# Performance work log

Hardware: AMD Instinct MI355X
Metric: run time of the kernel (lower is better)

Reference implementation:

```python
import jax, jax.numpy as jnp
import numpy as np

D_MODEL = 1024
N_HEADS = 16
D_V = D_MODEL // N_HEADS  # 64; o_proj maps d_model -> d_v (quirk of the source)
B, S = 4, 2048


def setup_inputs() -> dict:
    key = jax.random.key(0)
    ks = jax.random.split(key, 5)
    scale = 1.0 / np.sqrt(D_MODEL)
    return {
        "in_features": jax.random.normal(ks[0], (B, S, D_MODEL), dtype=jnp.float32),
        "Wq": jax.random.normal(ks[1], (D_MODEL, D_MODEL), dtype=jnp.float32) * scale,
        "Wk": jax.random.normal(ks[2], (D_MODEL, D_MODEL), dtype=jnp.float32) * scale,
        "Wv": jax.random.normal(ks[3], (D_MODEL, D_MODEL), dtype=jnp.float32) * scale,
        "Wo": jax.random.normal(ks[4], (D_V, D_MODEL), dtype=jnp.float32) * scale,
    }


def reference(in_features, Wq, Wk, Wv, Wo):
    # Linear(in, out): y = x @ W^T, no bias. NOTE: source never splits heads;
    # attention runs single-head over the full d_model dims.
    Q = jnp.einsum('bsd,ed->bse', in_features, Wq)  # [B,S,D]
    K = jnp.einsum('bsd,ed->bse', in_features, Wk)
    V = jnp.einsum('bsd,ed->bse', in_features, Wv)

    scores = jnp.einsum('bqd,bkd->bqk', Q, K)       # [B,S,S]
    causal = jnp.tril(jnp.ones((S, S), dtype=bool))  # True = keep
    # source applies -inf mask BEFORE scaling (equivalent result)
    scores = jnp.where(causal[None, :, :], scores, -jnp.inf)
    scores = scores / jnp.sqrt(jnp.float32(D_MODEL))  # K.size(-1) == d_model
    attn = jax.nn.softmax(scores, axis=-1)
    ctx = jnp.einsum('bqk,bkd->bqd', attn, V)        # [B,S,D]
    return jnp.einsum('bsd,vd->bsv', ctx, Wo)        # [B,S,D_V]
```

## Files before the change

### kernel.cpp

```cpp
#include <hip/hip_runtime.h>
#include <math.h>

typedef unsigned short u16;
typedef unsigned int u32;
typedef __attribute__((ext_vector_type(8))) short short8;
typedef __attribute__((ext_vector_type(4))) short short4v;
typedef __attribute__((ext_vector_type(4))) float f32x4;

#define BB 4
#define SS 2048
#define DD 1024
#define DV 64
#define NYU 1152
#define BS (BB * SS)
#define SCALE (1.0f / 32.0f)

__device__ __forceinline__ u16 f2bf(float f) {
    u32 u = __builtin_bit_cast(u32, f);
    u32 r = u + 0x7fffu + ((u >> 16) & 1u);
    return (u16)(r >> 16);
}
__device__ __forceinline__ float bf2f(u16 b) {
    return __builtin_bit_cast(float, (u32)b << 16);
}
__device__ __forceinline__ void storeC(float* p, float v) { *p = v; }
__device__ __forceinline__ void storeC(u16* p, float v) { *p = f2bf(v); }

__global__ __launch_bounds__(256) void prep(const float* __restrict__ x,
                                            const float* __restrict__ Wq,
                                            const float* __restrict__ Wk,
                                            const float* __restrict__ Wo,
                                            const float* __restrict__ Wv,
                                            u16* __restrict__ x16,
                                            u16* __restrict__ Wqt,
                                            u16* __restrict__ Wkt,
                                            float* __restrict__ wpart) {
    __shared__ float smem[64 * 128];
    const int b = blockIdx.x;
    const int tid = threadIdx.x;
    if (b < 8192) {
        int i = b * 256 + tid;
        f32x4 v = ((const f32x4*)x)[i];
        short4v o;
        o.x = (short)f2bf(v.x); o.y = (short)f2bf(v.y);
        o.z = (short)f2bf(v.z); o.w = (short)f2bf(v.w);
        ((short4v*)x16)[i] = o;
    } else if (b < 8704) {
        const int bb = b - 8192;
        const float* src = (bb >> 8) ? Wk : Wq;
        u16* dst = (bb >> 8) ? Wkt : Wqt;
        const int rem = bb & 255;
        const int e0 = (rem >> 4) * 64, d0 = (rem & 15) * 64;
        u16* t = (u16*)smem;
        const int g = tid >> 6, lane = tid & 63;
        for (int r = g; r < 64; r += 4)
            t[r * 72 + lane] = f2bf(src[(size_t)(e0 + r) * DD + d0 + lane]);
        __syncthreads();
        for (int r = g; r < 64; r += 4)
            dst[(size_t)(d0 + r) * DD + e0 + lane] = t[lane * 72 + r];
    } else {
        const int bb = b - 8704;
        const int echunk = (bb & 7) * 128;
        const int kc = bb >> 3, kbase = kc * 128;
        for (int idx = tid; idx < 64 * 128; idx += 256)
            smem[idx] = Wo[(size_t)(idx >> 7) * DD + kbase + (idx & 127)];
        __syncthreads();
        const int eo = echunk + (tid & 31) * 4;
        const int ob = (tid >> 5) * 8;
        float acc[8][4] = {};
        for (int k = 0; k < 128; ++k) {
            f32x4 wv = *(const f32x4*)&Wv[(size_t)(kbase + k) * DD + eo];
#pragma unroll
            for (int oi = 0; oi < 8; ++oi) {
                float s = smem[(ob + oi) * 128 + k];
                acc[oi][0] += s * wv.x; acc[oi][1] += s * wv.y;
                acc[oi][2] += s * wv.z; acc[oi][3] += s * wv.w;
            }
        }
#pragma unroll
        for (int oi = 0; oi < 8; ++oi)
            *(f32x4*)&wpart[((size_t)kc * 64 + ob + oi) * DD + eo] =
                (f32x4){acc[oi][0], acc[oi][1], acc[oi][2], acc[oi][3]};
    }
}

__global__ __launch_bounds__(256) void reduce_all(const float* __restrict__ Gpart,
                                                  const float* __restrict__ wpart,
                                                  u16* __restrict__ Wall2) {
    const int bx = blockIdx.x;
    const int e0 = threadIdx.x * 4;
    f32x4 s = (f32x4){0.f, 0.f, 0.f, 0.f};
    if (bx < 1024) {
#pragma unroll
        for (int kc = 0; kc < 4; ++kc)
            s += *(const f32x4*)&Gpart[(size_t)kc * DD * DD + (size_t)bx * DD + e0];
    } else if (bx < 1088) {
#pragma unroll
        for (int kc = 0; kc < 8; ++kc)
            s += *(const f32x4*)&wpart[((size_t)kc * 64 + bx - 1024) * DD + e0];
    }
    short4v ov;
    ov.x = (short)f2bf(s.x); ov.y = (short)f2bf(s.y);
    ov.z = (short)f2bf(s.z); ov.w = (short)f2bf(s.w);
    *(short4v*)&Wall2[(size_t)bx * DD + e0] = ov;
}

template <int TM, int TN, int WM, int WN, typename OutT, int MODE>
__global__ __launch_bounds__(WM * WN * 64) void gemm_nt_mfma(
    const u16* __restrict__ A, const u16* __restrict__ B, OutT* __restrict__ C,
    int lda, int ldb, int ldc, int K, long sA, long sB, long sC) {
    constexpr int NW = WM * WN;
    constexpr int CA = TM / 16;
    constexpr int CB = TN / 16;

    const int z = blockIdx.z;
    A += (size_t)z * sA;
    B += (size_t)z * sB;
    C += (size_t)z * sC;
    int m0, n0;
    if constexpr (MODE == 3) {
        const int b = blockIdx.x;
        const int r = b & 7, q = b >> 3;
        m0 = (r * 8 + q / 9) * TM;
        n0 = (q % 9) * TN;
    } else {
        m0 = blockIdx.y * TM;
        n0 = blockIdx.x * TN;
    }

    __shared__ u16 As[TM * 32];
    __shared__ u16 Bs[TN * 32];

    const int tid = threadIdx.x;
    const int w = tid >> 6, lane = tid & 63;
    const int wm = w / WN, wn = w % WN;
    const int lrow = lane >> 2;
    const int lcol = (lane & 3) * 8;
    const int m16 = lane & 15;
    const int kh = (lane >> 4) * 8;

    f32x4 acc[4][4];
#pragma unroll
    for (int i = 0; i < 4; ++i)
#pragma unroll
        for (int j = 0; j < 4; ++j) acc[i][j] = (f32x4){0.f, 0.f, 0.f, 0.f};

    for (int k0 = 0; k0 < K; k0 += 32) {
        for (int c = w; c < CA; c += NW) {
            const u16* g = A + (size_t)(m0 + c * 16 + lrow) * lda + k0 + lcol;
            __builtin_amdgcn_global_load_lds(
                (const __attribute__((address_space(1))) void*)g,
                (__attribute__((address_space(3))) void*)(&As[c * 512]), 16, 0, 0);
        }
        for (int c = w; c < CB; c += NW) {
            const u16* g = B + (size_t)(n0 + c * 16 + lrow) * ldb + k0 + lcol;
            __builtin_amdgcn_global_load_lds(
                (const __attribute__((address_space(1))) void*)g,
                (__attribute__((address_space(3))) void*)(&Bs[c * 512]), 16, 0, 0);
        }
        __syncthreads();

        short8 a[4], b[4];
#pragma unroll
        for (int i = 0; i < 4; ++i)
            a[i] = *(const short8*)&As[(wm * 64 + i * 16 + m16) * 32 + kh];
#pragma unroll
        for (int j = 0; j < 4; ++j)
            b[j] = *(const short8*)&Bs[(wn * 64 + j * 16 + m16) * 32 + kh];
#pragma unroll
        for (int i = 0; i < 4; ++i)
#pragma unroll
            for (int j = 0; j < 4; ++j)
                acc[i][j] = __builtin_amdgcn_mfma_f32_16x16x32_bf16(a[i], b[j], acc[i][j], 0, 0, 0);
        __syncthreads();
    }

    const int crow0 = m0 + wm * 64 + (lane >> 4) * 4;
    const int ccol0 = n0 + wn * 64 + m16;
#pragma unroll
    for (int i = 0; i < 4; ++i)
#pragma unroll
        for (int j = 0; j < 4; ++j)
#pragma unroll
            for (int r = 0; r < 4; ++r)
                storeC(&C[(size_t)(crow0 + i * 16 + r) * ldc + ccol0 + j * 16],
                       acc[i][j][r]);
}

__global__ __launch_bounds__(256) void transpose_u(const u16* __restrict__ YU,
                                                   u16* __restrict__ Ut) {
    __shared__ u16 t[64][72];
    const int s0 = blockIdx.x * 64;
    const int g = threadIdx.x >> 6, lane = threadIdx.x & 63;
    for (int r = g; r < 64; r += 4)
        t[r][lane] = YU[(size_t)(s0 + r) * NYU + 1024 + lane];
    __syncthreads();
    for (int r = g; r < 64; r += 4)
        Ut[(size_t)r * BS + s0 + lane] = t[lane][r];
}

__global__ __launch_bounds__(256) void scores_pv(const u16* __restrict__ YU,
                                                 const u16* __restrict__ x16,
                                                 const u16* __restrict__ Ut,
                                                 float* __restrict__ out,
                                                 float* __restrict__ Lacc) {
    const int b = blockIdx.x;
    const int r8 = b & 7;
    const int z = r8 >> 1;
    const int t = 2 * (b >> 3) + (r8 & 1);
    int y = (int)((sqrtf(8.f * t + 1.f) - 1.f) * 0.5f);
    while ((y + 1) * (y + 2) / 2 <= t) ++y;
    while (y * (y + 1) / 2 > t) --y;
    const int m0 = y * 128;
    const int n0 = (t - y * (y + 1) / 2) * 128;

    const u16* A = YU + (size_t)z * SS * NYU;
    const u16* B = x16 + (size_t)z * SS * DD;

    __shared__ u16 As[128 * 32];
    __shared__ u16 Bs[128 * 32];
    __shared__ u16 Ps[128 * 136];

    const int tid = threadIdx.x;
    const int w = tid >> 6, lane = tid & 63;
    const int wm = w >> 1, wn = w & 1;
    const int lrow = lane >> 2;
    const int lcol = (lane & 3) * 8;
    const int m16 = lane & 15;
    const int kh = (lane >> 4) * 8;

    f32x4 acc[4][4];
#pragma unroll
    for (int i = 0; i < 4; ++i)
#pragma unroll
        for (int j = 0; j < 4; ++j) acc[i][j] = (f32x4){0.f, 0.f, 0.f, 0.f};

    for (int k0 = 0; k0 < DD; k0 += 32) {
        for (int c = w; c < 8; c += 4) {
            const u16* g = A + (size_t)(m0 + c * 16 + lrow) * NYU + k0 + lcol;
            __builtin_amdgcn_global_load_lds(
                (const __attribute__((address_space(1))) void*)g,
                (__attribute__((address_space(3))) void*)(&As[c * 512]), 16, 0, 0);
        }
        for (int c = w; c < 8; c += 4) {
            const u16* g = B + (size_t)(n0 + c * 16 + lrow) * DD + k0 + lcol;
            __builtin_amdgcn_global_load_lds(
                (const __attribute__((address_space(1))) void*)g,
                (__attribute__((address_space(3))) void*)(&Bs[c * 512]), 16, 0, 0);
        }
        __syncthreads();

        short8 a[4], bb[4];
#pragma unroll
        for (int i = 0; i < 4; ++i)
            a[i] = *(const short8*)&As[(wm * 64 + i * 16 + m16) * 32 + kh];
#pragma unroll
        for (int j = 0; j < 4; ++j)
            bb[j] = *(const short8*)&Bs[(wn * 64 + j * 16 + m16) * 32 + kh];
#pragma unroll
        for (int i = 0; i < 4; ++i)
#pragma unroll
            for (int j = 0; j < 4; ++j)
                acc[i][j] = __builtin_amdgcn_mfma_f32_16x16x32_bf16(a[i], bb[j], acc[i][j], 0, 0, 0);
        __syncthreads();
    }

    const int rl0 = wm * 64 + (lane >> 4) * 4;
    const int cl0 = wn * 64 + m16;
#pragma unroll
    for (int i = 0; i < 4; ++i)
#pragma unroll
        for (int j = 0; j < 4; ++j)
#pragma unroll
            for (int r = 0; r < 4; ++r) {
                const int rl = rl0 + i * 16 + r;
                const int cl = cl0 + j * 16;
                float p = __expf(acc[i][j][r] * SCALE);
                Ps[rl * 136 + cl] = (n0 + cl <= m0 + rl) ? f2bf(p) : (u16)0;
            }
    __syncthreads();

    short8 ones8;
#pragma unroll
    for (int e = 0; e < 8; ++e) ones8[e] = (short)0x3F80;

    const u16* Utz = Ut + (size_t)z * SS + n0;
    f32x4 accO[2][4], accL[2];
#pragma unroll
    for (int i = 0; i < 2; ++i) {
        accL[i] = (f32x4){0.f, 0.f, 0.f, 0.f};
#pragma unroll
        for (int j = 0; j < 4; ++j) accO[i][j] = (f32x4){0.f, 0.f, 0.f, 0.f};
    }
#pragma unroll
    for (int ks = 0; ks < 4; ++ks) {
        const int k0 = ks * 32;
        short8 a[2], bb[4];
#pragma unroll
        for (int i = 0; i < 2; ++i)
            a[i] = *(const short8*)&Ps[(w * 32 + i * 16 + m16) * 136 + k0 + kh];
#pragma unroll
        for (int j = 0; j < 4; ++j)
            bb[j] = *(const short8*)&Utz[(size_t)(j * 16 + m16) * BS + k0 + kh];
#pragma unroll
        for (int i = 0; i < 2; ++i) {
#pragma unroll
            for (int j = 0; j < 4; ++j)
                accO[i][j] = __builtin_amdgcn_mfma_f32_16x16x32_bf16(a[i], bb[j], accO[i][j], 0, 0, 0);
            accL[i] = __builtin_amdgcn_mfma_f32_16x16x32_bf16(a[i], ones8, accL[i], 0, 0, 0);
        }
    }

    float* Oz = out + (size_t)z * SS * DV;
    float* Lz = Lacc + (size_t)z * SS;
    const int wrow = m0 + w * 32 + (lane >> 4) * 4;
#pragma unroll
    for (int i = 0; i < 2; ++i) {
#pragma unroll
        for (int j = 0; j < 4; ++j)
#pragma unroll
            for (int r = 0; r < 4; ++r)
                atomicAdd(&Oz[(size_t)(wrow + i * 16 + r) * DV + j * 16 + m16],
                          accO[i][j][r]);
        if (m16 == 0)
#pragma unroll
            for (int r = 0; r < 4; ++r)
                atomicAdd(&Lz[wrow + i * 16 + r], accL[i][r]);
    }
}

__global__ __launch_bounds__(256) void normalize(float* __restrict__ out,
                                                 const float* __restrict__ Lacc) {
    int i = blockIdx.x * 256 + threadIdx.x;
    f32x4 v = ((f32x4*)out)[i];
    const float inv = 1.f / Lacc[(i * 4) >> 6];
    v.x *= inv; v.y *= inv; v.z *= inv; v.w *= inv;
    ((f32x4*)out)[i] = v;
}

extern "C" void kernel_launch(void* const* d_in, const int* in_sizes, int n_in,
                              void* d_out, int out_size, void* d_ws, size_t ws_size,
                              hipStream_t stream) {
    const float* x  = (const float*)d_in[0];
    const float* Wq = (const float*)d_in[1];
    const float* Wk = (const float*)d_in[2];
    const float* Wv = (const float*)d_in[3];
    const float* Wo = (const float*)d_in[4];
    float* out = (float*)d_out;

    u16* x16   = (u16*)d_ws;
    u16* Wqt16 = x16 + (size_t)BB * SS * DD;
    u16* Wkt16 = Wqt16 + (size_t)DD * DD;
    u16* Wall2 = Wkt16 + (size_t)DD * DD;
    u16* YU    = Wall2 + (size_t)NYU * DD;
    u16* Ut    = YU + (size_t)BB * SS * NYU;
    float* wpart = (float*)(Ut + (size_t)DV * BS);
    float* Lacc  = wpart + (size_t)8 * 64 * DD;
    float* Gpart = (float*)YU;

    hipMemsetAsync(out, 0, (size_t)out_size * sizeof(float), stream);
    hipMemsetAsync(Lacc, 0, (size_t)BS * sizeof(float), stream);

    prep<<<dim3(8768), 256, 0, stream>>>(x, Wq, Wk, Wo, Wv, x16, Wqt16, Wkt16, wpart);

    gemm_nt_mfma<128, 128, 2, 2, float, 0><<<dim3(8, 8, 4), 256, 0, stream>>>(
        Wkt16, Wqt16, Gpart, DD, DD, DD, 256, 256, 256, (long)DD * DD);

    reduce_all<<<dim3(NYU), 256, 0, stream>>>(Gpart, wpart, Wall2);

    gemm_nt_mfma<128, 128, 2, 2, u16, 3><<<dim3(576), 256, 0, stream>>>(
        x16, Wall2, YU, DD, DD, NYU, DD, 0, 0, 0);

    transpose_u<<<dim3(BS / 64), 256, 0, stream>>>(YU, Ut);

    scores_pv<<<dim3(544), 256, 0, stream>>>(YU, x16, Ut, out, Lacc);

    normalize<<<dim3(out_size / 4 / 256), 256, 0, stream>>>(out, Lacc);
}
```

Measured before the change: 209.7 us.

## Fuse U transpose into projection GEMM epilogue and shrink attention tiles to 128x64

The separate transpose_u kernel is removed: the projection GEMM now uses 128x64 tiles with two waves, and the column tile that holds the U slice also writes its transposed bf16 values straight into Ut. scores_pv switches to 128x64 causal tiles with two waves, so fewer masked entries are computed near the diagonal, and it places the P buffer in a union with the staging buffers to save LDS. The reduce kernel no longer writes the unused padding rows. The trade-off is less operand reuse per tile, scattered 2-byte transposed stores, and twice as many blocks issuing atomics on the output.

```diff
diff --git a/kernel.cpp b/kernel.cpp
--- a/kernel.cpp
+++ b/kernel.cpp
@@ -94,7 +94,7 @@
 #pragma unroll
         for (int kc = 0; kc < 4; ++kc)
             s += *(const f32x4*)&Gpart[(size_t)kc * DD * DD + (size_t)bx * DD + e0];
-    } else if (bx < 1088) {
+    } else {
 #pragma unroll
         for (int kc = 0; kc < 8; ++kc)
             s += *(const f32x4*)&wpart[((size_t)kc * 64 + bx - 1024) * DD + e0];
@@ -108,7 +108,8 @@
 template <int TM, int TN, int WM, int WN, typename OutT, int MODE>
 __global__ __launch_bounds__(WM * WN * 64) void gemm_nt_mfma(
     const u16* __restrict__ A, const u16* __restrict__ B, OutT* __restrict__ C,
-    int lda, int ldb, int ldc, int K, long sA, long sB, long sC) {
+    int lda, int ldb, int ldc, int K, long sA, long sB, long sC,
+    u16* __restrict__ Utp) {
     constexpr int NW = WM * WN;
     constexpr int CA = TM / 16;
     constexpr int CB = TN / 16;
@@ -118,11 +119,11 @@
     B += (size_t)z * sB;
     C += (size_t)z * sC;
     int m0, n0;
-    if constexpr (MODE == 3) {
+    if constexpr (MODE == 4) {
         const int b = blockIdx.x;
         const int r = b & 7, q = b >> 3;
-        m0 = (r * 8 + q / 9) * TM;
-        n0 = (q % 9) * TN;
+        m0 = (r * 8 + q / 17) * TM;
+        n0 = (q % 17) * TN;
     } else {
         m0 = blockIdx.y * TM;
         n0 = blockIdx.x * TN;
@@ -182,24 +183,17 @@
 #pragma unroll
         for (int j = 0; j < 4; ++j)
 #pragma unroll
-            for (int r = 0; r < 4; ++r)
-                storeC(&C[(size_t)(crow0 + i * 16 + r) * ldc + ccol0 + j * 16],
-                       acc[i][j][r]);
-}
-
-__global__ __launch_bounds__(256) void transpose_u(const u16* __restrict__ YU,
-                                                   u16* __restrict__ Ut) {
-    __shared__ u16 t[64][72];
-    const int s0 = blockIdx.x * 64;
-    const int g = threadIdx.x >> 6, lane = threadIdx.x & 63;
-    for (int r = g; r < 64; r += 4)
-        t[r][lane] = YU[(size_t)(s0 + r) * NYU + 1024 + lane];
-    __syncthreads();
-    for (int r = g; r < 64; r += 4)
-        Ut[(size_t)r * BS + s0 + lane] = t[lane][r];
-}
-
-__global__ __launch_bounds__(256) void scores_pv(const u16* __restrict__ YU,
+            for (int r = 0; r < 4; ++r) {
+                const float v = acc[i][j][r];
+                storeC(&C[(size_t)(crow0 + i * 16 + r) * ldc + ccol0 + j * 16], v);
+                if constexpr (MODE == 4) {
+                    if (n0 == 1024)
+                        Utp[(size_t)(ccol0 + j * 16 - 1024) * BS + crow0 + i * 16 + r] = f2bf(v);
+                }
+            }
+}
+
+__global__ __launch_bounds__(128) void scores_pv(const u16* __restrict__ YU,
                                                  const u16* __restrict__ x16,
                                                  const u16* __restrict__ Ut,
                                                  float* __restrict__ out,
@@ -208,22 +202,22 @@
     const int r8 = b & 7;
     const int z = r8 >> 1;
     const int t = 2 * (b >> 3) + (r8 & 1);
-    int y = (int)((sqrtf(8.f * t + 1.f) - 1.f) * 0.5f);
-    while ((y + 1) * (y + 2) / 2 <= t) ++y;
-    while (y * (y + 1) / 2 > t) --y;
+    int y = (int)((sqrtf(4.f * t + 1.f) - 1.f) * 0.5f);
+    while ((y + 1) * (y + 2) <= t) ++y;
+    while (y * (y + 1) > t) --y;
     const int m0 = y * 128;
-    const int n0 = (t - y * (y + 1) / 2) * 128;
+    const int n0 = (t - y * (y + 1)) * 64;
 
     const u16* A = YU + (size_t)z * SS * NYU;
     const u16* B = x16 + (size_t)z * SS * DD;
 
-    __shared__ u16 As[128 * 32];
-    __shared__ u16 Bs[128 * 32];
-    __shared__ u16 Ps[128 * 136];
+    __shared__ union ShU {
+        struct { u16 As[128 * 32]; u16 Bs[64 * 32]; } s;
+        u16 Ps[128 * 72];
+    } sh;
 
     const int tid = threadIdx.x;
     const int w = tid >> 6, lane = tid & 63;
-    const int wm = w >> 1, wn = w & 1;
     const int lrow = lane >> 2;
     const int lcol = (lane & 3) * 8;
     const int m16 = lane & 15;
@@ -236,27 +230,27 @@
         for (int j = 0; j < 4; ++j) acc[i][j] = (f32x4){0.f, 0.f, 0.f, 0.f};
 
     for (int k0 = 0; k0 < DD; k0 += 32) {
-        for (int c = w; c < 8; c += 4) {
+        for (int c = w; c < 8; c += 2) {
             const u16* g = A + (size_t)(m0 + c * 16 + lrow) * NYU + k0 + lcol;
             __builtin_amdgcn_global_load_lds(
                 (const __attribute__((address_space(1))) void*)g,
-                (__attribute__((address_space(3))) void*)(&As[c * 512]), 16, 0, 0);
-        }
-        for (int c = w; c < 8; c += 4) {
+                (__attribute__((address_space(3))) void*)(&sh.s.As[c * 512]), 16, 0, 0);
+        }
+        for (int c = w; c < 4; c += 2) {
             const u16* g = B + (size_t)(n0 + c * 16 + lrow) * DD + k0 + lcol;
             __builtin_amdgcn_global_load_lds(
                 (const __attribute__((address_space(1))) void*)g,
-                (__attribute__((address_space(3))) void*)(&Bs[c * 512]), 16, 0, 0);
+                (__attribute__((address_space(3))) void*)(&sh.s.Bs[c * 512]), 16, 0, 0);
         }
         __syncthreads();
 
         short8 a[4], bb[4];
 #pragma unroll
         for (int i = 0; i < 4; ++i)
-            a[i] = *(const short8*)&As[(wm * 64 + i * 16 + m16) * 32 + kh];
-#pragma unroll
-        for (int j = 0; j < 4; ++j)
-            bb[j] = *(const short8*)&Bs[(wn * 64 + j * 16 + m16) * 32 + kh];
+            a[i] = *(const short8*)&sh.s.As[(w * 64 + i * 16 + m16) * 32 + kh];
+#pragma unroll
+        for (int j = 0; j < 4; ++j)
+            bb[j] = *(const short8*)&sh.s.Bs[(j * 16 + m16) * 32 + kh];
 #pragma unroll
         for (int i = 0; i < 4; ++i)
 #pragma unroll
@@ -265,8 +259,7 @@
         __syncthreads();
     }
 
-    const int rl0 = wm * 64 + (lane >> 4) * 4;
-    const int cl0 = wn * 64 + m16;
+    const int rl0 = w * 64 + (lane >> 4) * 4;
 #pragma unroll
     for (int i = 0; i < 4; ++i)
 #pragma unroll
@@ -274,9 +267,9 @@
 #pragma unroll
             for (int r = 0; r < 4; ++r) {
                 const int rl = rl0 + i * 16 + r;
-                const int cl = cl0 + j * 16;
+                const int cl = j * 16 + m16;
                 float p = __expf(acc[i][j][r] * SCALE);
-                Ps[rl * 136 + cl] = (n0 + cl <= m0 + rl) ? f2bf(p) : (u16)0;
+                sh.Ps[rl * 72 + cl] = (n0 + cl <= m0 + rl) ? f2bf(p) : (u16)0;
             }
     __syncthreads();
 
@@ -285,25 +278,25 @@
     for (int e = 0; e < 8; ++e) ones8[e] = (short)0x3F80;
 
     const u16* Utz = Ut + (size_t)z * SS + n0;
-    f32x4 accO[2][4], accL[2];
-#pragma unroll
-    for (int i = 0; i < 2; ++i) {
+    f32x4 accO[4][4], accL[4];
+#pragma unroll
+    for (int i = 0; i < 4; ++i) {
         accL[i] = (f32x4){0.f, 0.f, 0.f, 0.f};
 #pragma unroll
         for (int j = 0; j < 4; ++j) accO[i][j] = (f32x4){0.f, 0.f, 0.f, 0.f};
     }
 #pragma unroll
-    for (int ks = 0; ks < 4; ++ks) {
+    for (int ks = 0; ks < 2; ++ks) {
         const int k0 = ks * 32;
-        short8 a[2], bb[4];
-#pragma unroll
-        for (int i = 0; i < 2; ++i)
-            a[i] = *(const short8*)&Ps[(w * 32 + i * 16 + m16) * 136 + k0 + kh];
+        short8 a[4], bb[4];
+#pragma unroll
+        for (int i = 0; i < 4; ++i)
+            a[i] = *(const short8*)&sh.Ps[(w * 64 + i * 16 + m16) * 72 + k0 + kh];
 #pragma unroll
         for (int j = 0; j < 4; ++j)
             bb[j] = *(const short8*)&Utz[(size_t)(j * 16 + m16) * BS + k0 + kh];
 #pragma unroll
-        for (int i = 0; i < 2; ++i) {
+        for (int i = 0; i < 4; ++i) {
 #pragma unroll
             for (int j = 0; j < 4; ++j)
                 accO[i][j] = __builtin_amdgcn_mfma_f32_16x16x32_bf16(a[i], bb[j], accO[i][j], 0, 0, 0);
@@ -313,19 +306,19 @@
 
     float* Oz = out + (size_t)z * SS * DV;
     float* Lz = Lacc + (size_t)z * SS;
-    const int wrow = m0 + w * 32 + (lane >> 4) * 4;
-#pragma unroll
-    for (int i = 0; i < 2; ++i) {
+    const int wrow0 = m0 + w * 64 + (lane >> 4) * 4;
+#pragma unroll
+    for (int i = 0; i < 4; ++i) {
 #pragma unroll
         for (int j = 0; j < 4; ++j)
 #pragma unroll
             for (int r = 0; r < 4; ++r)
-                atomicAdd(&Oz[(size_t)(wrow + i * 16 + r) * DV + j * 16 + m16],
+                atomicAdd(&Oz[(size_t)(wrow0 + i * 16 + r) * DV + j * 16 + m16],
                           accO[i][j][r]);
         if (m16 == 0)
 #pragma unroll
             for (int r = 0; r < 4; ++r)
-                atomicAdd(&Lz[wrow + i * 16 + r], accL[i][r]);
+                atomicAdd(&Lz[wrow0 + i * 16 + r], accL[i][r]);
     }
 }
 
@@ -364,16 +357,14 @@
     prep<<<dim3(8768), 256, 0, stream>>>(x, Wq, Wk, Wo, Wv, x16, Wqt16, Wkt16, wpart);
 
     gemm_nt_mfma<128, 128, 2, 2, float, 0><<<dim3(8, 8, 4), 256, 0, stream>>>(
-        Wkt16, Wqt16, Gpart, DD, DD, DD, 256, 256, 256, (long)DD * DD);
-
-    reduce_all<<<dim3(NYU), 256, 0, stream>>>(Gpart, wpart, Wall2);
-
-    gemm_nt_mfma<128, 128, 2, 2, u16, 3><<<dim3(576), 256, 0, stream>>>(
-        x16, Wall2, YU, DD, DD, NYU, DD, 0, 0, 0);
-
-    transpose_u<<<dim3(BS / 64), 256, 0, stream>>>(YU, Ut);
-
-    scores_pv<<<dim3(544), 256, 0, stream>>>(YU, x16, Ut, out, Lacc);
+        Wkt16, Wqt16, Gpart, DD, DD, DD, 256, 256, 256, (long)DD * DD, nullptr);
+
+    reduce_all<<<dim3(1088), 256, 0, stream>>>(Gpart, wpart, Wall2);
+
+    gemm_nt_mfma<128, 64, 2, 1, u16, 4><<<dim3(1088), 128, 0, stream>>>(
+        x16, Wall2, YU, DD, DD, NYU, DD, 0, 0, 0, Ut);
+
+    scores_pv<<<dim3(1088), 128, 0, stream>>>(YU, x16, Ut, out, Lacc);
 
     normalize<<<dim3(out_size / 4 / 256), 256, 0, stream>>>(out, Lacc);
 }
```

Result: slower. 252.9 us (+20.6%).

## Fuse memsets into prep, fold U transpose into GEMM epilogue, union LDS

Applied to the files above, without the earlier changes.

Removes the two hipMemsetAsync calls by zeroing out and Lacc inside extra blocks of the prep kernel. Drops the separate transpose_u kernel by having the YU GEMM tiles that cover the U columns also write the transposed Ut copy from their epilogue. Also trims reduce_all to 1088 blocks, skipping the 64 zero-fill rows, and overlays the scores_pv As/Bs staging buffers with Ps in a shared-memory union to cut LDS use. The aim is fewer launches and less separate memory traffic. The cost is strided, uncoalesced Ut stores in the GEMM epilogue and possible stale data in the unwritten Wall2 rows, although the GEMM grid only reads columns up to 1088.

```diff
diff --git a/kernel.cpp b/kernel.cpp
--- a/kernel.cpp
+++ b/kernel.cpp
@@ -34,7 +34,9 @@
                                             u16* __restrict__ x16,
                                             u16* __restrict__ Wqt,
                                             u16* __restrict__ Wkt,
-                                            float* __restrict__ wpart) {
+                                            float* __restrict__ wpart,
+                                            float* __restrict__ out,
+                                            float* __restrict__ Lacc) {
     __shared__ float smem[64 * 128];
     const int b = blockIdx.x;
     const int tid = threadIdx.x;
@@ -58,7 +60,7 @@
         __syncthreads();
         for (int r = g; r < 64; r += 4)
             dst[(size_t)(d0 + r) * DD + e0 + lane] = t[lane * 72 + r];
-    } else {
+    } else if (b < 8768) {
         const int bb = b - 8704;
         const int echunk = (bb & 7) * 128;
         const int kc = bb >> 3, kbase = kc * 128;
@@ -81,6 +83,12 @@
         for (int oi = 0; oi < 8; ++oi)
             *(f32x4*)&wpart[((size_t)kc * 64 + ob + oi) * DD + eo] =
                 (f32x4){acc[oi][0], acc[oi][1], acc[oi][2], acc[oi][3]};
+    } else if (b < 9280) {
+        int i = (b - 8768) * 256 + tid;
+        ((f32x4*)out)[i] = (f32x4){0.f, 0.f, 0.f, 0.f};
+    } else {
+        int i = (b - 9280) * 256 + tid;
+        ((f32x4*)Lacc)[i] = (f32x4){0.f, 0.f, 0.f, 0.f};
     }
 }
 
@@ -94,7 +102,7 @@
 #pragma unroll
         for (int kc = 0; kc < 4; ++kc)
             s += *(const f32x4*)&Gpart[(size_t)kc * DD * DD + (size_t)bx * DD + e0];
-    } else if (bx < 1088) {
+    } else {
 #pragma unroll
         for (int kc = 0; kc < 8; ++kc)
             s += *(const f32x4*)&wpart[((size_t)kc * 64 + bx - 1024) * DD + e0];
@@ -108,7 +116,8 @@
 template <int TM, int TN, int WM, int WN, typename OutT, int MODE>
 __global__ __launch_bounds__(WM * WN * 64) void gemm_nt_mfma(
     const u16* __restrict__ A, const u16* __restrict__ B, OutT* __restrict__ C,
-    int lda, int ldb, int ldc, int K, long sA, long sB, long sC) {
+    int lda, int ldb, int ldc, int K, long sA, long sB, long sC,
+    u16* __restrict__ Utp) {
     constexpr int NW = WM * WN;
     constexpr int CA = TM / 16;
     constexpr int CB = TN / 16;
@@ -182,21 +191,14 @@
 #pragma unroll
         for (int j = 0; j < 4; ++j)
 #pragma unroll
-            for (int r = 0; r < 4; ++r)
-                storeC(&C[(size_t)(crow0 + i * 16 + r) * ldc + ccol0 + j * 16],
-                       acc[i][j][r]);
-}
-
-__global__ __launch_bounds__(256) void transpose_u(const u16* __restrict__ YU,
-                                                   u16* __restrict__ Ut) {
-    __shared__ u16 t[64][72];
-    const int s0 = blockIdx.x * 64;
-    const int g = threadIdx.x >> 6, lane = threadIdx.x & 63;
-    for (int r = g; r < 64; r += 4)
-        t[r][lane] = YU[(size_t)(s0 + r) * NYU + 1024 + lane];
-    __syncthreads();
-    for (int r = g; r < 64; r += 4)
-        Ut[(size_t)r * BS + s0 + lane] = t[lane][r];
+            for (int r = 0; r < 4; ++r) {
+                const float v = acc[i][j][r];
+                storeC(&C[(size_t)(crow0 + i * 16 + r) * ldc + ccol0 + j * 16], v);
+                if constexpr (MODE == 3) {
+                    if (n0 == 1024 && wn == 0)
+                        Utp[(size_t)(ccol0 + j * 16 - 1024) * BS + crow0 + i * 16 + r] = f2bf(v);
+                }
+            }
 }
 
 __global__ __launch_bounds__(256) void scores_pv(const u16* __restrict__ YU,
@@ -217,9 +219,10 @@
     const u16* A = YU + (size_t)z * SS * NYU;
     const u16* B = x16 + (size_t)z * SS * DD;
 
-    __shared__ u16 As[128 * 32];
-    __shared__ u16 Bs[128 * 32];
-    __shared__ u16 Ps[128 * 136];
+    __shared__ union ShU {
+        struct { u16 As[128 * 32]; u16 Bs[128 * 32]; } s;
+        u16 Ps[128 * 136];
+    } sh;
 
     const int tid = threadIdx.x;
     const int w = tid >> 6, lane = tid & 63;
@@ -240,23 +243,23 @@
             const u16* g = A + (size_t)(m0 + c * 16 + lrow) * NYU + k0 + lcol;
             __builtin_amdgcn_global_load_lds(
                 (const __attribute__((address_space(1))) void*)g,
-                (__attribute__((address_space(3))) void*)(&As[c * 512]), 16, 0, 0);
+                (__attribute__((address_space(3))) void*)(&sh.s.As[c * 512]), 16, 0, 0);
         }
         for (int c = w; c < 8; c += 4) {
             const u16* g = B + (size_t)(n0 + c * 16 + lrow) * DD + k0 + lcol;
             __builtin_amdgcn_global_load_lds(
                 (const __attribute__((address_space(1))) void*)g,
-                (__attribute__((address_space(3))) void*)(&Bs[c * 512]), 16, 0, 0);
+                (__attribute__((address_space(3))) void*)(&sh.s.Bs[c * 512]), 16, 0, 0);
         }
         __syncthreads();
 
         short8 a[4], bb[4];
 #pragma unroll
         for (int i = 0; i < 4; ++i)
-            a[i] = *(const short8*)&As[(wm * 64 + i * 16 + m16) * 32 + kh];
-#pragma unroll
-        for (int j = 0; j < 4; ++j)
-            bb[j] = *(const short8*)&Bs[(wn * 64 + j * 16 + m16) * 32 + kh];
+            a[i] = *(const short8*)&sh.s.As[(wm * 64 + i * 16 + m16) * 32 + kh];
+#pragma unroll
+        for (int j = 0; j < 4; ++j)
+            bb[j] = *(const short8*)&sh.s.Bs[(wn * 64 + j * 16 + m16) * 32 + kh];
 #pragma unroll
         for (int i = 0; i < 4; ++i)
 #pragma unroll
@@ -276,7 +279,7 @@
                 const int rl = rl0 + i * 16 + r;
                 const int cl = cl0 + j * 16;
                 float p = __expf(acc[i][j][r] * SCALE);
-                Ps[rl * 136 + cl] = (n0 + cl <= m0 + rl) ? f2bf(p) : (u16)0;
+                sh.Ps[rl * 136 + cl] = (n0 + cl <= m0 + rl) ? f2bf(p) : (u16)0;
             }
     __syncthreads();
 
@@ -298,7 +301,7 @@
         short8 a[2], bb[4];
 #pragma unroll
         for (int i = 0; i < 2; ++i)
-            a[i] = *(const short8*)&Ps[(w * 32 + i * 16 + m16) * 136 + k0 + kh];
+            a[i] = *(const short8*)&sh.Ps[(w * 32 + i * 16 + m16) * 136 + k0 + kh];
 #pragma unroll
         for (int j = 0; j < 4; ++j)
             bb[j] = *(const short8*)&Utz[(size_t)(j * 16 + m16) * BS + k0 + kh];
@@ -358,20 +361,16 @@
     float* Lacc  = wpart + (size_t)8 * 64 * DD;
     float* Gpart = (float*)YU;
 
-    hipMemsetAsync(out, 0, (size_t)out_size * sizeof(float), stream);
-    hipMemsetAsync(Lacc, 0, (size_t)BS * sizeof(float), stream);
-
-    prep<<<dim3(8768), 256, 0, stream>>>(x, Wq, Wk, Wo, Wv, x16, Wqt16, Wkt16, wpart);
+    prep<<<dim3(9288), 256, 0, stream>>>(x, Wq, Wk, Wo, Wv, x16, Wqt16, Wkt16,
+                                         wpart, out, Lacc);
 
     gemm_nt_mfma<128, 128, 2, 2, float, 0><<<dim3(8, 8, 4), 256, 0, stream>>>(
-        Wkt16, Wqt16, Gpart, DD, DD, DD, 256, 256, 256, (long)DD * DD);
-
-    reduce_all<<<dim3(NYU), 256, 0, stream>>>(Gpart, wpart, Wall2);
+        Wkt16, Wqt16, Gpart, DD, DD, DD, 256, 256, 256, (long)DD * DD, nullptr);
+
+    reduce_all<<<dim3(1088), 256, 0, stream>>>(Gpart, wpart, Wall2);
 
     gemm_nt_mfma<128, 128, 2, 2, u16, 3><<<dim3(576), 256, 0, stream>>>(
-        x16, Wall2, YU, DD, DD, NYU, DD, 0, 0, 0);
-
-    transpose_u<<<dim3(BS / 64), 256, 0, stream>>>(YU, Ut);
+        x16, Wall2, YU, DD, DD, NYU, DD, 0, 0, 0, Ut);
 
     scores_pv<<<dim3(544), 256, 0, stream>>>(YU, x16, Ut, out, Lacc);
 
```

Result: faster. 204.4 us (-2.5%).
